# Optimization experiments

Measured on AMD Instinct MI355X. Metric: run time of the kernel, lower is better.

Reference implementation:

```python
import jax, jax.numpy as jnp
import numpy as np

POOLING_COUNTS = [15, 8, 8, 8]
N = 128


def _build_entries():
    """Replicates SparseMaxPool.__init__: per step (kernel, pool_stride, i_idx, j_idx)."""
    entries = []
    stride, offset = 1, 0
    for ci, c in enumerate(POOLING_COUNTS):
        for k in range(c):
            offset += stride
            # pooler layout: first block all MaxPool1d(2,1); later blocks start with MaxPool1d(3,2)
            kernel = 3 if (ci > 0 and k == 0) else 2
            pstride = 2 if kernel == 3 else 1
            i = np.arange(0, N - offset, stride)
            j = np.arange(offset, N, stride)
            entries.append((kernel, pstride, i, j))
        stride *= 2
    return entries

_ENTRIES = _build_entries()


def _maxpool1d(x, kernel, stride):
    # x: [B, D, L] -> [B, D, (L-kernel)//stride + 1]
    L = x.shape[-1]
    out = (L - kernel) // stride + 1
    slices = [x[..., t : t + (out - 1) * stride + 1 : stride] for t in range(kernel)]
    y = slices[0]
    for s in slices[1:]:
        y = jnp.maximum(y, s)
    return y


def setup_inputs() -> dict:
    key = jax.random.key(0)
    x = jax.random.normal(key, (16, 256, N), dtype=jnp.float32)
    return {"x": x}


def reference(x):
    B, D, Nv = x.shape
    map2d = jnp.zeros((B, D, N, N), dtype=x.dtype)
    diag = np.arange(N)
    map2d = map2d.at[:, :, diag, diag].set(x)
    for kernel, pstride, i, j in _ENTRIES:
        x = _maxpool1d(x, kernel, pstride)
        map2d = map2d.at[:, :, i, j].set(x)
    return map2d
```

## Files before the change

kernel.cpp:

```cpp
#include <hip/hip_runtime.h>


#define NN 128
#define SLICE_ELEMS (NN * NN)

__device__ __forceinline__ float entry_val(const float* __restrict__ buf, int r, int c) {
    int o = c - r;
    int w = o + 1;
    int wcl = w < 1 ? 1 : w;
    int k = 31 - __clz(wcl);
    int p2 = 1 << k;
    int lb = 129 * k - (p2 - 1);
    int d2 = wcl - p2;
    int oc = o < 1 ? 1 : o;
    int t = 31 - __clz(oc);
    int sh = t - 3;
    sh = sh < 0 ? 0 : (sh > 3 ? 3 : sh);
    int m = (1 << sh) - 1;
    bool valid = (o >= 0) & ((o & m) == m) & ((r & m) == 0);
    float v = fmaxf(buf[lb + r], buf[lb + r + d2]);
    return valid ? v : 0.0f;
}

__global__ __launch_bounds__(256) void sparse_maxpool_kernel(
        const float* __restrict__ x, float* __restrict__ out) {
    __shared__ float buf[1040];
    const int tid = threadIdx.x;
    const int slice = blockIdx.x;

    if (tid < NN) buf[tid] = x[(size_t)slice * NN + tid];
    __syncthreads();

    int base_prev = 0, base_cur = NN;
    #pragma unroll
    for (int k = 1; k <= 7; ++k) {
        int half = 1 << (k - 1);
        int len = (NN + 1) - (1 << k);
        if (tid < len)
            buf[base_cur + tid] = fmaxf(buf[base_prev + tid], buf[base_prev + tid + half]);
        __syncthreads();
        base_prev = base_cur;
        base_cur += len;
    }

    float4* __restrict__ out_s = reinterpret_cast<float4*>(out + (size_t)slice * SLICE_ELEMS);
    #pragma unroll
    for (int it = 0; it < 16; ++it) {
        int idx = it * 256 + tid;
        int r = idx >> 5;
        int c0 = (idx & 31) << 2;
        float4 v;
        v.x = entry_val(buf, r, c0);
        v.y = entry_val(buf, r, c0 + 1);
        v.z = entry_val(buf, r, c0 + 2);
        v.w = entry_val(buf, r, c0 + 3);
        out_s[idx] = v;
    }
}

extern "C" void kernel_launch(void* const* d_in, const int* in_sizes, int n_in,
                              void* d_out, int out_size, void* d_ws, size_t ws_size,
                              hipStream_t stream) {
    const float* x = (const float*)d_in[0];
    float* out = (float*)d_out;
    const int slices = in_sizes[0] / NN;
    sparse_maxpool_kernel<<<dim3(slices), dim3(256), 0, stream>>>(x, out);
}
```

Measured before the change: 257.9 us.

## Zero-fill output with float4 stores then scatter only valid sparse entries

Replaces the per-element validity computation over the full 128x128 map with a bulk float4 zero fill, followed by scattered scalar stores of only the valid diagonal-band entries, enumerated per pooling group. This removes most of the index math and LDS reads done for entries that end up zero. The shared buffer is also shrunk. The cost is a second, uncoalesced write pass over a small subset of the output, and the two passes must be correctly ordered for the same addresses.

After: 260.1 us. About the same (+0.9%).

```diff
diff --git a/kernel.cpp b/kernel.cpp
--- a/kernel.cpp
+++ b/kernel.cpp
@@ -4,33 +4,30 @@
 #define NN 128
 #define SLICE_ELEMS (NN * NN)
 
-__device__ __forceinline__ float entry_val(const float* __restrict__ buf, int r, int c) {
-    int o = c - r;
+__device__ __forceinline__ void win_params(int o, int& lb, int& d2) {
     int w = o + 1;
-    int wcl = w < 1 ? 1 : w;
-    int k = 31 - __clz(wcl);
+    int k = 31 - __clz(w);
     int p2 = 1 << k;
-    int lb = 129 * k - (p2 - 1);
-    int d2 = wcl - p2;
-    int oc = o < 1 ? 1 : o;
-    int t = 31 - __clz(oc);
-    int sh = t - 3;
-    sh = sh < 0 ? 0 : (sh > 3 ? 3 : sh);
-    int m = (1 << sh) - 1;
-    bool valid = (o >= 0) & ((o & m) == m) & ((r & m) == 0);
-    float v = fmaxf(buf[lb + r], buf[lb + r + d2]);
-    return valid ? v : 0.0f;
+    lb = 129 * k - (p2 - 1);
+    d2 = w - p2;
 }
 
 __global__ __launch_bounds__(256) void sparse_maxpool_kernel(
         const float* __restrict__ x, float* __restrict__ out) {
-    __shared__ float buf[1040];
+    __shared__ float buf[784];
     const int tid = threadIdx.x;
     const int slice = blockIdx.x;
+    float* __restrict__ out_s = out + (size_t)slice * SLICE_ELEMS;
 
     if (tid < NN) buf[tid] = x[(size_t)slice * NN + tid];
+
+    float4 z = make_float4(0.f, 0.f, 0.f, 0.f);
+    float4* __restrict__ o4 = reinterpret_cast<float4*>(out_s);
+    #pragma unroll
+    for (int it = 0; it < 16; ++it)
+        o4[it * 256 + tid] = z;
+
     __syncthreads();
-
     int base_prev = 0, base_cur = NN;
     #pragma unroll
     for (int k = 1; k <= 7; ++k) {
@@ -43,18 +40,41 @@
         base_cur += len;
     }
 
-    float4* __restrict__ out_s = reinterpret_cast<float4*>(out + (size_t)slice * SLICE_ELEMS);
-    #pragma unroll
-    for (int it = 0; it < 16; ++it) {
-        int idx = it * 256 + tid;
-        int r = idx >> 5;
-        int c0 = (idx & 31) << 2;
-        float4 v;
-        v.x = entry_val(buf, r, c0);
-        v.y = entry_val(buf, r, c0 + 1);
-        v.z = entry_val(buf, r, c0 + 2);
-        v.w = entry_val(buf, r, c0 + 3);
-        out_s[idx] = v;
+    {
+        int o = tid & 15, lb, d2;
+        win_params(o, lb, d2);
+        int r0 = tid >> 4;
+        #pragma unroll
+        for (int jj = 0; jj < 8; ++jj) {
+            int r = r0 + 16 * jj;
+            if (r + o < NN)
+                out_s[r * 129 + o] = fmaxf(buf[lb + r], buf[lb + r + d2]);
+        }
+    }
+    {
+        int o = 17 + 2 * (tid & 7), lb, d2;
+        win_params(o, lb, d2);
+        int r0 = 2 * (tid >> 3);
+        #pragma unroll
+        for (int jj = 0; jj < 2; ++jj) {
+            int r = r0 + 64 * jj;
+            if (r + o < NN)
+                out_s[r * 129 + o] = fmaxf(buf[lb + r], buf[lb + r + d2]);
+        }
+    }
+    {
+        int o = 35 + 4 * (tid & 7), lb, d2;
+        win_params(o, lb, d2);
+        int r = 4 * (tid >> 3);
+        if (r + o < NN)
+            out_s[r * 129 + o] = fmaxf(buf[lb + r], buf[lb + r + d2]);
+    }
+    {
+        int o = 71 + 8 * (tid & 7), lb, d2;
+        win_params(o, lb, d2);
+        int r = 8 * (tid >> 3);
+        if (r + o < NN)
+            out_s[r * 129 + o] = fmaxf(buf[lb + r], buf[lb + r + d2]);
     }
 }
 
```
